# Kernel optimization log

Measured on AMD Instinct MI355X. Metric: run time of the kernel, lower is better.

## Reference

```python
import jax, jax.numpy as jnp
import numpy as np

TEMP = 0.05
DIAG_PENALTY = 1e12
EPS = 1e-8  # matches torch F.cosine_similarity eps


def setup_inputs() -> dict:
    key = jax.random.key(0)
    x = jax.random.normal(key, (8192, 768), dtype=jnp.float32)
    return {"x": x}


def reference(x):
    n = x.shape[0]
    # labels: swap adjacent pairs -> i - (i%2)*2 + 1  (i.e. i XOR 1)
    idx = jnp.arange(n)
    labels = idx - (idx % 2) * 2 + 1
    # cosine similarity matrix via normalize + GEMM (same math as broadcasted
    # F.cosine_similarity: dot(x_i, x_j) / (max(||x_i||,eps) * max(||x_j||,eps)))
    norms = jnp.maximum(jnp.linalg.norm(x, axis=-1, keepdims=True), EPS)
    xn = x / norms
    sim = xn @ xn.T                                   # [N, N]
    sim = sim - jnp.eye(n, dtype=sim.dtype) * DIAG_PENALTY
    logits = sim / TEMP
    # mean cross-entropy with stable log-softmax
    logp = jax.nn.log_softmax(logits, axis=-1)
    loss = -jnp.mean(jnp.take_along_axis(logp, labels[:, None], axis=-1))
    return loss
```

## Files before the change

kernel.cpp:

```cpp
#include <hip/hip_runtime.h>
#include <hip/hip_bf16.h>

#define N 8192
#define D 768
#define TEMP_INV 20.0f
#define NTILES 2080

typedef __attribute__((ext_vector_type(4))) float f32x4;
typedef __attribute__((ext_vector_type(4))) int i32x4;
typedef __attribute__((ext_vector_type(8))) int i32x8;

#define SCALE1 0x7F7F7F7F


__global__ __launch_bounds__(256) void norm_kernel(
    const float* __restrict__ x, unsigned char* __restrict__ xn,
    float* __restrict__ rowsum) {
  int t = threadIdx.x, w = t >> 6, lane = t & 63;
  int row = blockIdx.x * 4 + w;
  const float4* xr = (const float4*)(x + (size_t)row * D);
  float4 v[3];
  v[0] = xr[lane];
  v[1] = xr[lane + 64];
  v[2] = xr[lane + 128];
  float ss = 0.0f;
#pragma unroll
  for (int i = 0; i < 3; ++i)
    ss += v[i].x * v[i].x + v[i].y * v[i].y + v[i].z * v[i].z + v[i].w * v[i].w;
#pragma unroll
  for (int m = 32; m; m >>= 1) ss += __shfl_xor(ss, m);
  float inv = 1.0f / fmaxf(sqrtf(ss), 1e-8f);
  unsigned int* xo = (unsigned int*)(xn + (size_t)row * D);
#pragma unroll
  for (int i = 0; i < 3; ++i) {
    int p = __builtin_amdgcn_cvt_pk_fp8_f32(v[i].x * inv, v[i].y * inv, 0, false);
    p = __builtin_amdgcn_cvt_pk_fp8_f32(v[i].z * inv, v[i].w * inv, p, true);
    xo[lane + 64 * i] = p;
  }
  if (t < 4) rowsum[blockIdx.x * 4 + t] = 0.0f;
}

__global__ __launch_bounds__(256, 4) void sim_kernel(
    const unsigned char* __restrict__ xn, float* __restrict__ rowsum,
    float* __restrict__ pos) {
  static const short stbase[37] = {
      0, 36, 100, 164, 228, 292, 356, 420,
      484, 520, 584, 648, 712, 776, 840,
      904, 940, 1004, 1068, 1132, 1196,
      1260, 1296, 1360, 1424, 1488,
      1552, 1588, 1652, 1716,
      1780, 1816, 1880,
      1944, 1980,
      2044, 2080};
  static const char sti[36] = {0,0,0,0,0,0,0,0, 1,1,1,1,1,1,1, 2,2,2,2,2,2,
                               3,3,3,3,3, 4,4,4,4, 5,5,5, 6,6, 7};
  static const char stj[36] = {0,1,2,3,4,5,6,7, 1,2,3,4,5,6,7, 2,3,4,5,6,7,
                               3,4,5,6,7, 4,5,6,7, 5,6,7, 6,7, 7};
  int b = blockIdx.x;
  int p = 260 * (b & 7) + (b >> 3);
  int s = 0;
  while ((int)stbase[s + 1] <= p) ++s;
  int wofs = p - stbase[s];
  int SI = sti[s], SJ = stj[s];
  int bi, bj;
  if (SI == SJ) {
    int di = 0, cum = 0;
    while (wofs >= cum + (8 - di)) { cum += 8 - di; ++di; }
    bi = SI * 8 + di;
    bj = SI * 8 + di + (wofs - cum);
  } else {
    bi = SI * 8 + (wofs >> 3);
    bj = SJ * 8 + (wofs & 7);
  }

  __shared__ i32x4 As4[128 * 8];
  __shared__ i32x4 Bs4[128 * 8];

  int t = threadIdx.x;
  int w = t >> 6, lane = t & 63;
  int q = lane >> 4, cl = lane & 15;
  int wm = w >> 1, wn = w & 1;

  f32x4 acc[4][4] = {};

  int ulog = (((t & 7) ^ ((t >> 3) & 7))) * 16;
  const unsigned char* Ab = xn + (size_t)(bi * 128 + (t >> 3)) * D + ulog;
  const unsigned char* Bb = xn + (size_t)(bj * 128 + (t >> 3)) * D + ulog;

  int u0 = (2 * q) ^ (cl & 7);
  int u1 = u0 ^ 1;

  for (int kc = 0; kc < 6; ++kc) {
    int k0 = kc * 128;
#pragma unroll
    for (int rr = 0; rr < 4; ++rr) {
      __builtin_amdgcn_global_load_lds(
          (const __attribute__((address_space(1))) unsigned int*)(Ab + (size_t)(rr * 32) * D + k0),
          (__attribute__((address_space(3))) unsigned int*)(As4 + rr * 256 + t), 16, 0, 0);
      __builtin_amdgcn_global_load_lds(
          (const __attribute__((address_space(1))) unsigned int*)(Bb + (size_t)(rr * 32) * D + k0),
          (__attribute__((address_space(3))) unsigned int*)(Bs4 + rr * 256 + t), 16, 0, 0);
    }
    __syncthreads();

    union Frag { i32x8 v8; struct { i32x4 lo, hi; } pr; };
    Frag a[4], bb[4];
#pragma unroll
    for (int m = 0; m < 4; ++m) {
      int rowb = (wm * 64 + m * 16 + cl) * 8;
      a[m].pr.lo = As4[rowb + u0];
      a[m].pr.hi = As4[rowb + u1];
    }
#pragma unroll
    for (int n = 0; n < 4; ++n) {
      int rowb = (wn * 64 + n * 16 + cl) * 8;
      bb[n].pr.lo = Bs4[rowb + u0];
      bb[n].pr.hi = Bs4[rowb + u1];
    }
#pragma unroll
    for (int m = 0; m < 4; ++m)
#pragma unroll
      for (int n = 0; n < 4; ++n)
        acc[m][n] = __builtin_amdgcn_mfma_scale_f32_16x16x128_f8f6f4(
            a[m].v8, bb[n].v8, acc[m][n], 0, 0, 0, SCALE1, 0, SCALE1);
    __syncthreads();
  }

  int gi0 = bi * 128 + wm * 64;
  int gj0 = bj * 128 + wn * 64;

  float rowp[4][4] = {};
  float colp[4] = {};

  if (bi == bj) {
#pragma unroll
    for (int m = 0; m < 4; ++m)
#pragma unroll
      for (int n = 0; n < 4; ++n)
#pragma unroll
        for (int r = 0; r < 4; ++r) {
          float sv = acc[m][n][r];
          int row = gi0 + m * 16 + q * 4 + r;
          int col = gj0 + n * 16 + cl;
          float e = __expf(TEMP_INV * sv - 20.0f);
          if (col == row) e = 0.0f;
          if (col == (row ^ 1)) pos[row] = TEMP_INV * sv;
          rowp[m][r] += e;
        }
  } else {
#pragma unroll
    for (int m = 0; m < 4; ++m)
#pragma unroll
      for (int n = 0; n < 4; ++n)
#pragma unroll
        for (int r = 0; r < 4; ++r) {
          float e = __expf(TEMP_INV * acc[m][n][r] - 20.0f);
          rowp[m][r] += e;
          colp[n] += e;
        }
  }

#pragma unroll
  for (int m = 0; m < 4; ++m)
#pragma unroll
    for (int r = 0; r < 4; ++r) {
      float v = rowp[m][r];
      v += __shfl_xor(v, 1);
      v += __shfl_xor(v, 2);
      v += __shfl_xor(v, 4);
      v += __shfl_xor(v, 8);
      if (cl == 0) atomicAdd(&rowsum[gi0 + m * 16 + q * 4 + r], v);
    }
  if (bi != bj) {
#pragma unroll
    for (int n = 0; n < 4; ++n) {
      float v = colp[n];
      v += __shfl_xor(v, 16);
      v += __shfl_xor(v, 32);
      if (q == 0) atomicAdd(&rowsum[gj0 + n * 16 + cl], v);
    }
  }
}

__global__ __launch_bounds__(1024) void loss_kernel(
    const float* __restrict__ rowsum, const float* __restrict__ pos,
    float* __restrict__ out) {
  int t = threadIdx.x;
  const float4* r4 = (const float4*)rowsum;
  const float4* p4 = (const float4*)pos;
  float acc = 0.0f;
#pragma unroll
  for (int it = 0; it < 2; ++it) {
    int i = t + it * 1024;
    float4 r = r4[i], pp = p4[i];
    acc += 80.0f + __logf(r.x) + __logf(r.y) + __logf(r.z) + __logf(r.w)
           - pp.x - pp.y - pp.z - pp.w;
  }
#pragma unroll
  for (int m = 32; m; m >>= 1) acc += __shfl_xor(acc, m);
  __shared__ float wsum[16];
  if ((t & 63) == 0) wsum[t >> 6] = acc;
  __syncthreads();
  if (t == 0) {
    float tot = 0.0f;
#pragma unroll
    for (int i = 0; i < 16; ++i) tot += wsum[i];
    out[0] = tot / (float)N;
  }
}

extern "C" void kernel_launch(void* const* d_in, const int* in_sizes, int n_in,
                              void* d_out, int out_size, void* d_ws, size_t ws_size,
                              hipStream_t stream) {
  const float* x = (const float*)d_in[0];
  float* rowsum = (float*)d_ws;
  float* pos = rowsum + N;
  unsigned char* xn = (unsigned char*)(rowsum + 2 * N + 16);

  norm_kernel<<<N / 4, 256, 0, stream>>>(x, xn, rowsum);
  sim_kernel<<<NTILES, 256, 0, stream>>>(xn, rowsum, pos);
  loss_kernel<<<1, 1024, 0, stream>>>(rowsum, pos, (float*)d_out);
}
```

Measured before the change: 124.4 us.

## Double-buffer LDS tiles in sim kernel to overlap loads with MFMA

Splits the A/B shared tiles into two buffers and prefetches the next K-chunk with global_load_lds while the current chunk's MFMAs run. Each step then needs only one waitcnt plus barrier instead of a load, sync, compute, sync sequence. Shared memory per block doubles to 64KB and launch bounds drop to 2 blocks per CU, which lowers occupancy. There is a possible hazard: the barrier after each step's compute is the only thing stopping a wave from overwriting a buffer that other waves are still reading, and the LDS reads are only ordered by sched_barrier.

```diff
diff --git a/kernel.cpp b/kernel.cpp
--- a/kernel.cpp
+++ b/kernel.cpp
@@ -40,7 +40,7 @@
   if (t < 4) rowsum[blockIdx.x * 4 + t] = 0.0f;
 }
 
-__global__ __launch_bounds__(256, 4) void sim_kernel(
+__global__ __launch_bounds__(256, 2) void sim_kernel(
     const unsigned char* __restrict__ xn, float* __restrict__ rowsum,
     float* __restrict__ pos) {
   static const short stbase[37] = {
@@ -73,8 +73,8 @@
     bj = SJ * 8 + (wofs & 7);
   }
 
-  __shared__ i32x4 As4[128 * 8];
-  __shared__ i32x4 Bs4[128 * 8];
+  __shared__ i32x4 As4[2][128 * 8];
+  __shared__ i32x4 Bs4[2][128 * 8];
 
   int t = threadIdx.x;
   int w = t >> 6, lane = t & 63;
@@ -90,32 +90,41 @@
   int u0 = (2 * q) ^ (cl & 7);
   int u1 = u0 ^ 1;
 
-  for (int kc = 0; kc < 6; ++kc) {
-    int k0 = kc * 128;
+  auto stage = [&](int buf, int k0) {
 #pragma unroll
     for (int rr = 0; rr < 4; ++rr) {
       __builtin_amdgcn_global_load_lds(
           (const __attribute__((address_space(1))) unsigned int*)(Ab + (size_t)(rr * 32) * D + k0),
-          (__attribute__((address_space(3))) unsigned int*)(As4 + rr * 256 + t), 16, 0, 0);
+          (__attribute__((address_space(3))) unsigned int*)(&As4[buf][rr * 256 + t]), 16, 0, 0);
       __builtin_amdgcn_global_load_lds(
           (const __attribute__((address_space(1))) unsigned int*)(Bb + (size_t)(rr * 32) * D + k0),
-          (__attribute__((address_space(3))) unsigned int*)(Bs4 + rr * 256 + t), 16, 0, 0);
-    }
-    __syncthreads();
+          (__attribute__((address_space(3))) unsigned int*)(&Bs4[buf][rr * 256 + t]), 16, 0, 0);
+    }
+  };
+
+  stage(0, 0);
+  asm volatile("s_waitcnt vmcnt(0)" ::: "memory");
+  __builtin_amdgcn_s_barrier();
+  __builtin_amdgcn_sched_barrier(0);
+
+#pragma unroll
+  for (int kc = 0; kc < 6; ++kc) {
+    const int cur = kc & 1;
+    if (kc < 5) stage(cur ^ 1, (kc + 1) * 128);
 
     union Frag { i32x8 v8; struct { i32x4 lo, hi; } pr; };
     Frag a[4], bb[4];
 #pragma unroll
     for (int m = 0; m < 4; ++m) {
       int rowb = (wm * 64 + m * 16 + cl) * 8;
-      a[m].pr.lo = As4[rowb + u0];
-      a[m].pr.hi = As4[rowb + u1];
+      a[m].pr.lo = As4[cur][rowb + u0];
+      a[m].pr.hi = As4[cur][rowb + u1];
     }
 #pragma unroll
     for (int n = 0; n < 4; ++n) {
       int rowb = (wn * 64 + n * 16 + cl) * 8;
-      bb[n].pr.lo = Bs4[rowb + u0];
-      bb[n].pr.hi = Bs4[rowb + u1];
+      bb[n].pr.lo = Bs4[cur][rowb + u0];
+      bb[n].pr.hi = Bs4[cur][rowb + u1];
     }
 #pragma unroll
     for (int m = 0; m < 4; ++m)
@@ -123,7 +132,12 @@
       for (int n = 0; n < 4; ++n)
         acc[m][n] = __builtin_amdgcn_mfma_scale_f32_16x16x128_f8f6f4(
             a[m].v8, bb[n].v8, acc[m][n], 0, 0, 0, SCALE1, 0, SCALE1);
-    __syncthreads();
+
+    if (kc < 5) {
+      asm volatile("s_waitcnt vmcnt(0)" ::: "memory");
+      __builtin_amdgcn_s_barrier();
+      __builtin_amdgcn_sched_barrier(0);
+    }
   }
 
   int gi0 = bi * 128 + wm * 64;
```

After: 136.2 us. 9.5% more time.
